# Kernel optimization log

Hardware: AMD Instinct MI355X
Metric: run time of the kernel (lower is better)

## Reference

```python
import jax, jax.numpy as jnp
import numpy as np


def group_norm(x, g, b, groups, eps=1e-5):
    # x: (B, C, H, W), PyTorch GroupNorm semantics
    B, C, H, W = x.shape
    xr = x.reshape(B, groups, -1)
    m = xr.mean(-1, keepdims=True)
    v = xr.var(-1, keepdims=True)
    xn = ((xr - m) * jax.lax.rsqrt(v + eps)).reshape(B, C, H, W)
    return xn * g[:, None, None] + b[:, None, None]


def mamba(xs, in_w, conv_w, conv_b, xproj_w, dt_w, dt_b, A_log, D, out_w):
    # Standard Mamba block: in_proj -> causal depthwise conv -> SiLU ->
    # x_proj -> softplus(dt_proj) -> selective scan -> gate -> out_proj.
    Bsz, L, d = xs.shape
    di = in_w.shape[0] // 2
    r = dt_w.shape[1]
    n = A_log.shape[1]
    K = conv_w.shape[1]
    xz = xs @ in_w.T                           # (B, L, 2*di)
    xpart, z = xz[..., :di], xz[..., di:]
    xp = jnp.pad(xpart, ((0, 0), (K - 1, 0), (0, 0)))  # causal pad
    xc = conv_b + sum(xp[:, k:k + L, :] * conv_w[:, k] for k in range(K))
    xc = jax.nn.silu(xc)
    proj = xc @ xproj_w.T                      # (B, L, r + 2n)
    dt = proj[..., :r]
    Bm = proj[..., r:r + n]
    Cm = proj[..., r + n:]
    delta = jax.nn.softplus(dt @ dt_w.T + dt_b)   # (B, L, di)
    A = -jnp.exp(A_log)                            # (di, n)
    dA = jnp.exp(jnp.einsum('bld,dn->bldn', delta, A))
    dBu = jnp.einsum('bld,bln,bld->bldn', delta, Bm, xc)

    def step(h, inp):
        dA_t, dBu_t, C_t = inp
        h = dA_t * h + dBu_t                  # (B, di, n)
        return h, jnp.einsum('bdn,bn->bd', h, C_t)

    h0 = jnp.zeros((Bsz, di, n), xs.dtype)
    _, ys = jax.lax.scan(step, h0, (jnp.moveaxis(dA, 1, 0), jnp.moveaxis(dBu, 1, 0), jnp.moveaxis(Cm, 1, 0)))
    y = jnp.moveaxis(ys, 0, 1) + D * xc
    y = y * jax.nn.silu(z)
    return y @ out_w.T


def setup_inputs() -> dict:
    def nrm(i, shape, s=0.05):
        return jax.random.normal(jax.random.fold_in(jax.random.key(0), i), shape, dtype=jnp.float32) * s

    f32 = jnp.float32
    C = 128
    di, r, n = 256, 8, 16          # spa mamba: d_model=128, expand=2
    di2, r2 = 64, 2                # spe mamba: d_model=32
    A1 = jnp.log(jnp.broadcast_to(jnp.arange(1, n + 1, dtype=f32), (di, n)))
    A2 = jnp.log(jnp.broadcast_to(jnp.arange(1, n + 1, dtype=f32), (di2, n)))
    return {
        'x': nrm(0, (2, C, 64, 64), 1.0),
        'pe_w': nrm(1, (C, C)), 'pe_b': jnp.zeros((C,), f32),
        'pe_gn_g': jnp.ones((C,), f32), 'pe_gn_b': jnp.zeros((C,), f32),
        'spa_in_w': nrm(2, (2 * di, C)),
        'spa_conv_w': nrm(3, (di, 4)), 'spa_conv_b': jnp.zeros((di,), f32),
        'spa_xproj_w': nrm(4, (r + 2 * n, di)),
        'spa_dt_w': nrm(5, (di, r)), 'spa_dt_b': jnp.full((di,), -2.0, f32),
        'spa_Alog': A1, 'spa_D': jnp.ones((di,), f32),
        'spa_out_w': nrm(6, (C, di)),
        'spa_gn_g': jnp.ones((C,), f32), 'spa_gn_b': jnp.zeros((C,), f32),
        'spe_in_w': nrm(7, (2 * di2, 32)),
        'spe_conv_w': nrm(8, (di2, 4)), 'spe_conv_b': jnp.zeros((di2,), f32),
        'spe_xproj_w': nrm(9, (r2 + 2 * n, di2)),
        'spe_dt_w': nrm(10, (di2, r2)), 'spe_dt_b': jnp.full((di2,), -2.0, f32),
        'spe_Alog': A2, 'spe_D': jnp.ones((di2,), f32),
        'spe_out_w': nrm(11, (32, di2)),
        'spe_gn_g': jnp.ones((C,), f32), 'spe_gn_b': jnp.zeros((C,), f32),
        'fuse_w': jnp.full((2,), 0.5, f32),
        'cls_w': nrm(12, (10, C)), 'cls_b': jnp.zeros((10,), f32),
        'ref_dw_w': nrm(13, (C, 1, 3, 3)),
        'ref_gn_g': jnp.ones((C,), f32), 'ref_gn_b': jnp.zeros((C,), f32),
        'ref_pw_w': nrm(14, (1, C)), 'ref_pw_b': jnp.zeros((1,), f32),
        'alpha': jnp.asarray(1e-4, f32),
    }


def reference(x, pe_w, pe_b, pe_gn_g, pe_gn_b, spa_in_w, spa_conv_w, spa_conv_b, spa_xproj_w, spa_dt_w, spa_dt_b, spa_Alog, spa_D, spa_out_w, spa_gn_g, spa_gn_b, spe_in_w, spe_conv_w, spe_conv_b, spe_xproj_w, spe_dt_w, spe_dt_b, spe_Alog, spe_D, spe_out_w, spe_gn_g, spe_gn_b, fuse_w, cls_w, cls_b, ref_dw_w, ref_gn_g, ref_gn_b, ref_pw_w, ref_pw_b, alpha):
    B, _, H, W = x.shape
    # patch embedding: 1x1 conv + GroupNorm + SiLU
    h1 = jnp.einsum('bchw,oc->bohw', x, pe_w) + pe_b[:, None, None]
    h1 = jax.nn.silu(group_norm(h1, pe_gn_g, pe_gn_b, 4))
    # SpaMamba: scan over flattened spatial tokens (B, H*W, C)
    seq = h1.transpose(0, 2, 3, 1).reshape(B, H * W, -1)
    y = mamba(seq, spa_in_w, spa_conv_w, spa_conv_b, spa_xproj_w, spa_dt_w, spa_dt_b, spa_Alog, spa_D, spa_out_w)
    y = y.reshape(B, H, W, -1).transpose(0, 3, 1, 2)
    spa = jax.nn.silu(group_norm(y, spa_gn_g, spa_gn_b, 4)) + h1
    # SpeMamba: token_num=4, group_channel_num=32, channel_num=128 (no pad)
    seq2 = h1.transpose(0, 2, 3, 1).reshape(B * H * W, 4, 32)
    y2 = mamba(seq2, spe_in_w, spe_conv_w, spe_conv_b, spe_xproj_w, spe_dt_w, spe_dt_b, spe_Alog, spe_D, spe_out_w)
    y2 = y2.reshape(B, H, W, -1).transpose(0, 3, 1, 2)
    spe = h1 + jax.nn.silu(group_norm(y2, spe_gn_g, spe_gn_b, 4))
    # attention-weighted fusion + residual (BothMamba, use_att=True)
    wts = jax.nn.softmax(fuse_w)
    feat = spa * wts[0] + spe * wts[1] + h1
    # classifier head (1x1 conv)
    logits = jnp.einsum('bchw,oc->bohw', feat, cls_w) + cls_b[:, None, None]
    # BoundaryAwareLogitRefiner
    edge = jax.lax.conv_general_dilated(feat, ref_dw_w, (1, 1), ((1, 1), (1, 1)), feature_group_count=feat.shape[1], dimension_numbers=('NCHW', 'OIHW', 'NCHW'))
    edge = jax.nn.silu(group_norm(edge, ref_gn_g, ref_gn_b, 4))
    edge = jax.nn.sigmoid(jnp.einsum('bchw,oc->bohw', edge, ref_pw_w) + ref_pw_b[:, None, None])
    local = jax.lax.reduce_window(logits, 0.0, jax.lax.add, (1, 1, 3, 3), (1, 1, 1, 1), ((0, 0), (0, 0), (1, 1), (1, 1))) / 9.0  # count_include_pad=True
    return logits + alpha * (1.0 - edge) * (local - logits)
```

## Files before the change

### kernel.cpp

```cpp
#include <hip/hip_runtime.h>
#include <math.h>

#define DEV __device__ __forceinline__

DEV float sigm(float x){ return 1.f/(1.f+__expf(-x)); }
DEV float siluf(float x){ return x * sigm(x); }
DEV float softplusf(float x){ return x > 20.f ? x : log1pf(__expf(x)); }

static constexpr float NG = 131072.0f;

static constexpr size_t WS_H1    = 0;
static constexpr size_t WS_H1PRE = 1048576;
static constexpr size_t WS_XC    = 2097152;
static constexpr size_t WS_ZSIL  = 4194304;
static constexpr size_t WS_XZ    = 6291456;
static constexpr size_t WS_LOG   = 8650752;
static constexpr size_t WS_Y     = 10485760;
static constexpr size_t WS_QB    = 12582912;
static constexpr size_t WS_HSB   = 13631488;
static constexpr size_t WS_Y2    = 14155776;
static constexpr size_t WS_FEAT  = 15204352;
static constexpr size_t WS_STATS = 16252928;
static constexpr size_t WS_PEWT  = 16253056;
static constexpr size_t WS_INWT  = WS_PEWT  + 16384;
static constexpr size_t WS_OUTWT = WS_INWT  + 65536;

__global__ void __launch_bounds__(256)
k_red(const float* __restrict__ part, float* __restrict__ outS, int half){
  __shared__ float red[4];
  int b = blockIdx.x >> 3, j = blockIdx.x & 7;
  float s = 0.f;
  for (int i = b*half + threadIdx.x; i < (b+1)*half; i += 256)
    s += part[(size_t)i*8 + j];
  s += __shfl_xor(s,1); s += __shfl_xor(s,2); s += __shfl_xor(s,4);
  s += __shfl_xor(s,8); s += __shfl_xor(s,16); s += __shfl_xor(s,32);
  if ((threadIdx.x & 63) == 0) red[threadIdx.x>>6] = s;
  __syncthreads();
  if (threadIdx.x == 0) outS[b*8+j] = red[0]+red[1]+red[2]+red[3];
}

__global__ void __launch_bounds__(256)
k_transpose(const float* __restrict__ pe_w, const float* __restrict__ in_w,
            const float* __restrict__ out_w,
            float* __restrict__ peT, float* __restrict__ inT,
            float* __restrict__ outT){
  int i0 = blockIdx.x*256 + threadIdx.x;
  int nt = gridDim.x*256;
  for (int k = i0; k < 128*128; k += nt){ int r = k >> 7, c = k & 127; peT[c*128 + r] = pe_w[k]; }
  for (int k = i0; k < 512*128; k += nt){ int r = k >> 7, c = k & 127; inT[c*512 + r] = in_w[k]; }
  for (int k = i0; k < 128*256; k += nt){ int r = k >> 8, c = k & 255; outT[c*128 + r] = out_w[k]; }
}

__global__ void __launch_bounds__(256)
k_pe(const float* __restrict__ x, const float* __restrict__ peT,
     const float* __restrict__ pe_b, float* __restrict__ h1pre,
     float* __restrict__ part){
  __shared__ float As[16][36];
  __shared__ float Bs[16][64];
  __shared__ float red1[2][4], red2[2][4];
  int tid = threadIdx.x;
  int bx = blockIdx.x, by = blockIdx.y;
  int m0 = bx*32, n0 = by*64;
  int b = m0 >> 12, pl0 = m0 & 4095;
  int tx = tid & 15, ty = tid >> 4;
  float acc[2][4];
  #pragma unroll
  for (int i = 0; i < 2; i++)
    #pragma unroll
    for (int j = 0; j < 4; j++) acc[i][j] = 0.f;
  for (int k0 = 0; k0 < 128; k0 += 16){
    if (tid < 128){
      int k = tid >> 3, mm = (tid & 7)*4;
      float4 a = *(const float4*)(x + ((size_t)b*128 + k0+k)*4096 + pl0 + mm);
      *(float4*)&As[k][mm] = a;
    }
    {
      int k = tid >> 4, n = (tid & 15)*4;
      *(float4*)&Bs[k][n] = *(const float4*)(peT + (size_t)(k0+k)*128 + n0+n);
    }
    __syncthreads();
    #pragma unroll
    for (int k = 0; k < 16; k++){
      float2 av = *(const float2*)&As[k][ty*2];
      float4 bv = *(const float4*)&Bs[k][tx*4];
      acc[0][0] += av.x*bv.x; acc[0][1] += av.x*bv.y; acc[0][2] += av.x*bv.z; acc[0][3] += av.x*bv.w;
      acc[1][0] += av.y*bv.x; acc[1][1] += av.y*bv.y; acc[1][2] += av.y*bv.z; acc[1][3] += av.y*bv.w;
    }
    __syncthreads();
  }
  float4 bias = *(const float4*)(pe_b + n0 + tx*4);
  float s1 = 0.f, s2 = 0.f;
  #pragma unroll
  for (int i = 0; i < 2; i++){
    float4 st;
    st.x = acc[i][0]+bias.x; st.y = acc[i][1]+bias.y;
    st.z = acc[i][2]+bias.z; st.w = acc[i][3]+bias.w;
    s1 += st.x+st.y+st.z+st.w;
    s2 += st.x*st.x + st.y*st.y + st.z*st.z + st.w*st.w;
    *(float4*)(h1pre + (size_t)(m0 + ty*2 + i)*128 + n0 + tx*4) = st;
  }
  s1 += __shfl_xor(s1,1);  s2 += __shfl_xor(s2,1);
  s1 += __shfl_xor(s1,2);  s2 += __shfl_xor(s2,2);
  s1 += __shfl_xor(s1,4);  s2 += __shfl_xor(s2,4);
  s1 += __shfl_xor(s1,16); s2 += __shfl_xor(s2,16);
  s1 += __shfl_xor(s1,32); s2 += __shfl_xor(s2,32);
  int lane = tid & 63, w = tid >> 6;
  if ((lane & 55) == 0){
    int gl = (lane >> 3) & 1;
    red1[gl][w] = s1; red2[gl][w] = s2;
  }
  __syncthreads();
  if (tid < 8){
    int gg = tid >> 1, which = tid & 1;
    int gl = gg - by*2;
    float v = 0.f;
    if (gl == 0 || gl == 1){
      v = which ? (red2[gl][0]+red2[gl][1]+red2[gl][2]+red2[gl][3])
                : (red1[gl][0]+red1[gl][1]+red1[gl][2]+red1[gl][3]);
    }
    int pblk = b*256 + (bx & 127) + by*128;
    part[(size_t)pblk*8 + tid] = v;
  }
}

__global__ void __launch_bounds__(256)
k_xz(const float* __restrict__ h1pre, const float* __restrict__ inT,
     const float* __restrict__ stats, const float* __restrict__ gng,
     const float* __restrict__ gnb, float* __restrict__ h1,
     float* __restrict__ xz, float* __restrict__ zsil){
  __shared__ float As[16][68];
  __shared__ float Bs[16][64];
  int tid = threadIdx.x;
  int m0 = blockIdx.x*64, n0 = blockIdx.y*64;
  int tx = tid & 15, ty = tid >> 4;
  float acc[4][4];
  #pragma unroll
  for (int i = 0; i < 4; i++)
    #pragma unroll
    for (int j = 0; j < 4; j++) acc[i][j] = 0.f;
  for (int k0 = 0; k0 < 128; k0 += 16){
    {
      int m = tid >> 2, kk = (tid & 3)*4;
      int pixm = m0 + m, c0 = k0 + kk;
      int bb = pixm >> 12, g = c0 >> 5;
      float4 a = *(const float4*)(h1pre + (size_t)pixm*128 + c0);
      float mu = stats[(bb*4+g)*2] * (1.f/NG);
      float var = stats[(bb*4+g)*2+1] * (1.f/NG) - mu*mu;
      float rs = rsqrtf(var + 1e-5f);
      float4 gg = *(const float4*)(gng + c0);
      float4 gb = *(const float4*)(gnb + c0);
      float4 v;
      v.x = siluf((a.x-mu)*rs*gg.x + gb.x);
      v.y = siluf((a.y-mu)*rs*gg.y + gb.y);
      v.z = siluf((a.z-mu)*rs*gg.z + gb.z);
      v.w = siluf((a.w-mu)*rs*gg.w + gb.w);
      As[kk+0][m] = v.x; As[kk+1][m] = v.y; As[kk+2][m] = v.z; As[kk+3][m] = v.w;
      if (blockIdx.y == 0) *(float4*)(h1 + (size_t)pixm*128 + c0) = v;
    }
    {
      int k = tid >> 4, n = (tid & 15)*4;
      *(float4*)&Bs[k][n] = *(const float4*)(inT + (size_t)(k0+k)*512 + n0+n);
    }
    __syncthreads();
    #pragma unroll
    for (int k = 0; k < 16; k++){
      float4 av = *(const float4*)&As[k][ty*4];
      float4 bv = *(const float4*)&Bs[k][tx*4];
      acc[0][0] += av.x*bv.x; acc[0][1] += av.x*bv.y; acc[0][2] += av.x*bv.z; acc[0][3] += av.x*bv.w;
      acc[1][0] += av.y*bv.x; acc[1][1] += av.y*bv.y; acc[1][2] += av.y*bv.z; acc[1][3] += av.y*bv.w;
      acc[2][0] += av.z*bv.x; acc[2][1] += av.z*bv.y; acc[2][2] += av.z*bv.z; acc[2][3] += av.z*bv.w;
      acc[3][0] += av.w*bv.x; acc[3][1] += av.w*bv.y; acc[3][2] += av.w*bv.z; acc[3][3] += av.w*bv.w;
    }
    __syncthreads();
  }
  if (n0 < 256){
    #pragma unroll
    for (int i = 0; i < 4; i++){
      float4 st; st.x = acc[i][0]; st.y = acc[i][1]; st.z = acc[i][2]; st.w = acc[i][3];
      *(float4*)(xz + (size_t)(m0 + ty*4 + i)*512 + n0 + tx*4) = st;
    }
  } else {
    #pragma unroll
    for (int i = 0; i < 4; i++){
      float4 st;
      st.x = siluf(acc[i][0]); st.y = siluf(acc[i][1]);
      st.z = siluf(acc[i][2]); st.w = siluf(acc[i][3]);
      *(float4*)(zsil + (size_t)(m0 + ty*4 + i)*256 + (n0-256) + tx*4) = st;
    }
  }
}

__global__ void __launch_bounds__(256)
k_conv(const float* __restrict__ xz, const float* __restrict__ cw,
       const float* __restrict__ cb, float* __restrict__ xc){
  int idx = blockIdx.x*256 + threadIdx.x;
  int d = idx & 255;
  int l = (idx >> 8) & 4095;
  int b = idx >> 20;
  float v = cb[d];
  #pragma unroll
  for (int k = 0; k < 4; k++){
    int ls = l - 3 + k;
    if (ls >= 0) v += xz[(size_t)(b*4096 + ls)*512 + d] * cw[d*4 + k];
  }
  xc[idx] = siluf(v);
}

__global__ void __launch_bounds__(256)
k_proj(const float* __restrict__ xc, const float* __restrict__ xpw,
       float* __restrict__ proj){
  __shared__ float As[32][33];
  int tid = threadIdx.x;
  int t = tid & 31;
  int jg = tid >> 5;
  int tok0 = blockIdx.x * 32;
  float acc[5];
  #pragma unroll
  for (int j = 0; j < 5; j++) acc[j] = 0.f;
  for (int k0 = 0; k0 < 256; k0 += 32){
    {
      int m = tid >> 3, kk = (tid & 7)*4;
      float4 a = *(const float4*)(xc + (size_t)(tok0+m)*256 + k0+kk);
      As[kk+0][m]=a.x; As[kk+1][m]=a.y; As[kk+2][m]=a.z; As[kk+3][m]=a.w;
    }
    __syncthreads();
    #pragma unroll
    for (int k4 = 0; k4 < 8; k4++){
      float a0 = As[k4*4+0][t];
      float a1 = As[k4*4+1][t];
      float a2 = As[k4*4+2][t];
      float a3 = As[k4*4+3][t];
      #pragma unroll
      for (int j = 0; j < 5; j++){
        float4 w = *(const float4*)(xpw + (size_t)(jg*5+j)*256 + k0 + k4*4);
        acc[j] += a0*w.x + a1*w.y + a2*w.z + a3*w.w;
      }
    }
    __syncthreads();
  }
  float* pr = proj + (size_t)(tok0+t)*40 + jg*5;
  #pragma unroll
  for (int j = 0; j < 5; j++) pr[j] = acc[j];
}

__global__ void __launch_bounds__(256)
k_scan1(const float* __restrict__ proj, const float* __restrict__ xc,
        const float* __restrict__ dtw, const float* __restrict__ dtb,
        const float* __restrict__ Alog, float* __restrict__ P,
        float* __restrict__ Q){
  int blk = blockIdx.x;
  int dblk = blk & 3;
  int bc = blk >> 2;
  int b = bc >> 7, chunk = bc & 127;
  int tid = threadIdx.x;
  int dl = tid >> 2, ng = tid & 3;
  int d = dblk*64 + dl;
  float4 a4 = *(const float4*)(Alog + (size_t)d*16 + ng*4);
  float An[4] = {-__expf(a4.x), -__expf(a4.y), -__expf(a4.z), -__expf(a4.w)};
  const float4* wr = (const float4*)(dtw + (size_t)d*8);
  float4 w0 = wr[0], w1 = wr[1];
  float bd = dtb[d];
  float Pv[4] = {1.f,1.f,1.f,1.f}, Qv[4] = {0.f,0.f,0.f,0.f};
  size_t row0 = (size_t)(b*4096 + chunk*32);
  for (int l = 0; l < 32; l++){
    size_t r = row0 + l;
    const float4* pr4 = (const float4*)(proj + r*40);
    float4 p0 = pr4[0], p1 = pr4[1];
    float4 bm = pr4[2+ng];
    float dv = softplusf(bd + p0.x*w0.x + p0.y*w0.y + p0.z*w0.z + p0.w*w0.w
                            + p1.x*w1.x + p1.y*w1.y + p1.z*w1.z + p1.w*w1.w);
    float xv = xc[r*256 + d];
    float dBx = dv*xv;
    float bmv[4] = {bm.x, bm.y, bm.z, bm.w};
    #pragma unroll
    for (int k = 0; k < 4; k++){
      float a = __expf(dv*An[k]);
      Qv[k] = a*Qv[k] + bmv[k]*dBx;
      Pv[k] *= a;
    }
  }
  size_t o = (size_t)bc*4096 + dblk*1024 + tid*4;
  float4 pv; pv.x=Pv[0]; pv.y=Pv[1]; pv.z=Pv[2]; pv.w=Pv[3];
  float4 qv; qv.x=Qv[0]; qv.y=Qv[1]; qv.z=Qv[2]; qv.w=Qv[3];
  *(float4*)(P + o) = pv;
  *(float4*)(Q + o) = qv;
}

__global__ void __launch_bounds__(256)
k_scan2(const float* __restrict__ P, const float* __restrict__ Q,
        float* __restrict__ hs){
  __shared__ float Ps[128][33], Qs[128][33];
  int tid = threadIdx.x;
  int b = blockIdx.x >> 7;
  int dn0 = (blockIdx.x & 127) * 32;
  for (int i = tid; i < 128*8; i += 256){
    int ch = i >> 3, c4 = (i & 7)*4;
    size_t g = (size_t)(b*128+ch)*4096 + dn0 + c4;
    float4 p = *(const float4*)(P + g);
    float4 q = *(const float4*)(Q + g);
    Ps[ch][c4]=p.x; Ps[ch][c4+1]=p.y; Ps[ch][c4+2]=p.z; Ps[ch][c4+3]=p.w;
    Qs[ch][c4]=q.x; Qs[ch][c4+1]=q.y; Qs[ch][c4+2]=q.z; Qs[ch][c4+3]=q.w;
  }
  __syncthreads();
  int lane = tid & 63, wv = tid >> 6;
  for (int rep = 0; rep < 8; rep++){
    int c = wv*8 + rep;
    float p0 = Ps[2*lane][c],   q0 = Qs[2*lane][c];
    float p1 = Ps[2*lane+1][c], q1 = Qs[2*lane+1][c];
    float p = p0*p1;
    float q = p1*q0 + q1;
    #pragma unroll
    for (int off = 1; off < 64; off <<= 1){
      float pp = __shfl_up(p, off);
      float qp = __shfl_up(q, off);
      if (lane >= off){ q = p*qp + q; p = p*pp; }
    }
    float hprev = __shfl_up(q, 1);
    if (lane == 0) hprev = 0.f;
    Ps[2*lane][c]   = hprev;
    Ps[2*lane+1][c] = p0*hprev + q0;
  }
  __syncthreads();
  for (int i = tid; i < 128*8; i += 256){
    int ch = i >> 3, c4 = (i & 7)*4;
    size_t g = (size_t)(b*128+ch)*4096 + dn0 + c4;
    float4 h;
    h.x = Ps[ch][c4]; h.y = Ps[ch][c4+1]; h.z = Ps[ch][c4+2]; h.w = Ps[ch][c4+3];
    *(float4*)(hs + g) = h;
  }
}

__global__ void __launch_bounds__(256)
k_scan3(const float* __restrict__ proj, const float* __restrict__ xc,
        const float* __restrict__ zsil, const float* __restrict__ dtw,
        const float* __restrict__ dtb, const float* __restrict__ Alog,
        const float* __restrict__ Dv, const float* __restrict__ hs,
        float* __restrict__ y){
  int blk = blockIdx.x;
  int dblk = blk & 3;
  int bc = blk >> 2;
  int b = bc >> 7, chunk = bc & 127;
  int tid = threadIdx.x;
  int dl = tid >> 2, ng = tid & 3;
  int d = dblk*64 + dl;
  float4 a4 = *(const float4*)(Alog + (size_t)d*16 + ng*4);
  float An[4] = {-__expf(a4.x), -__expf(a4.y), -__expf(a4.z), -__expf(a4.w)};
  const float4* wr = (const float4*)(dtw + (size_t)d*8);
  float4 w0 = wr[0], w1 = wr[1];
  float bd = dtb[d];
  float Dd = Dv[d];
  float h[4];
  {
    size_t o = (size_t)bc*4096 + dblk*1024 + tid*4;
    float4 hv = *(const float4*)(hs + o);
    h[0]=hv.x; h[1]=hv.y; h[2]=hv.z; h[3]=hv.w;
  }
  size_t row0 = (size_t)(b*4096 + chunk*32);
  for (int l = 0; l < 32; l++){
    size_t r = row0 + l;
    const float4* pr4 = (const float4*)(proj + r*40);
    float4 p0 = pr4[0], p1 = pr4[1];
    float4 bm = pr4[2+ng];
    float4 cm = pr4[6+ng];
    float dv = softplusf(bd + p0.x*w0.x + p0.y*w0.y + p0.z*w0.z + p0.w*w0.w
                            + p1.x*w1.x + p1.y*w1.y + p1.z*w1.z + p1.w*w1.w);
    float xv = xc[r*256 + d];
    float dBx = dv*xv;
    float bmv[4] = {bm.x, bm.y, bm.z, bm.w};
    float cmv[4] = {cm.x, cm.y, cm.z, cm.w};
    float ys = 0.f;
    #pragma unroll
    for (int k = 0; k < 4; k++){
      float a = __expf(dv*An[k]);
      h[k] = a*h[k] + bmv[k]*dBx;
      ys += h[k]*cmv[k];
    }
    ys += __shfl_xor(ys, 1);
    ys += __shfl_xor(ys, 2);
    if (ng == 0){
      float zv = zsil[r*256 + d];
      y[r*256 + d] = (ys + Dd*xv) * zv;
    }
  }
}

__global__ void __launch_bounds__(256)
k_outproj(const float* __restrict__ y, const float* __restrict__ outT,
          float* __restrict__ yproj, float* __restrict__ part){
  __shared__ float As[16][36];
  __shared__ float Bs[16][64];
  __shared__ float red1[2][4], red2[2][4];
  int tid = threadIdx.x;
  int bx = blockIdx.x, by = blockIdx.y;
  int m0 = bx*32, n0 = by*64;
  int b = m0 >> 12;
  int tx = tid & 15, ty = tid >> 4;
  float acc[2][4];
  #pragma unroll
  for (int i = 0; i < 2; i++)
    #pragma unroll
    for (int j = 0; j < 4; j++) acc[i][j] = 0.f;
  for (int k0 = 0; k0 < 256; k0 += 16){
    if (tid < 128){
      int m = tid >> 2, kk = (tid & 3)*4;
      float4 a = *(const float4*)(y + (size_t)(m0+m)*256 + k0+kk);
      As[kk+0][m] = a.x; As[kk+1][m] = a.y; As[kk+2][m] = a.z; As[kk+3][m] = a.w;
    }
    {
      int k = tid >> 4, n = (tid & 15)*4;
      *(float4*)&Bs[k][n] = *(const float4*)(outT + (size_t)(k0+k)*128 + n0+n);
    }
    __syncthreads();
    #pragma unroll
    for (int k = 0; k < 16; k++){
      float2 av = *(const float2*)&As[k][ty*2];
      float4 bv = *(const float4*)&Bs[k][tx*4];
      acc[0][0] += av.x*bv.x; acc[0][1] += av.x*bv.y; acc[0][2] += av.x*bv.z; acc[0][3] += av.x*bv.w;
      acc[1][0] += av.y*bv.x; acc[1][1] += av.y*bv.y; acc[1][2] += av.y*bv.z; acc[1][3] += av.y*bv.w;
    }
    __syncthreads();
  }
  float s1 = 0.f, s2 = 0.f;
  #pragma unroll
  for (int i = 0; i < 2; i++){
    float4 st; st.x = acc[i][0]; st.y = acc[i][1]; st.z = acc[i][2]; st.w = acc[i][3];
    s1 += st.x+st.y+st.z+st.w;
    s2 += st.x*st.x + st.y*st.y + st.z*st.z + st.w*st.w;
    *(float4*)(yproj + (size_t)(m0 + ty*2 + i)*128 + n0 + tx*4) = st;
  }
  s1 += __shfl_xor(s1,1);  s2 += __shfl_xor(s2,1);
  s1 += __shfl_xor(s1,2);  s2 += __shfl_xor(s2,2);
  s1 += __shfl_xor(s1,4);  s2 += __shfl_xor(s2,4);
  s1 += __shfl_xor(s1,16); s2 += __shfl_xor(s2,16);
  s1 += __shfl_xor(s1,32); s2 += __shfl_xor(s2,32);
  int lane = tid & 63, w = tid >> 6;
  if ((lane & 55) == 0){
    int gl = (lane >> 3) & 1;
    red1[gl][w] = s1; red2[gl][w] = s2;
  }
  __syncthreads();
  if (tid < 8){
    int gg = tid >> 1, which = tid & 1;
    int gl = gg - by*2;
    float v = 0.f;
    if (gl == 0 || gl == 1){
      v = which ? (red2[gl][0]+red2[gl][1]+red2[gl][2]+red2[gl][3])
                : (red1[gl][0]+red1[gl][1]+red1[gl][2]+red1[gl][3]);
    }
    int pblk = b*256 + (bx & 127) + by*128;
    part[(size_t)pblk*8 + tid] = v;
  }
}

__global__ void __launch_bounds__(256)
k_spe_a(const float* __restrict__ h1, const float* __restrict__ in_w,
        const float* __restrict__ conv_w, const float* __restrict__ conv_b,
        float* __restrict__ xc2, float* __restrict__ xc2T,
        float* __restrict__ zsil2){
  __shared__ float s_in[4][128];
  int tid = threadIdx.x;
  int w = tid >> 6, lane = tid & 63;
  float wx[32], wz[32];
  {
    const float4* rx = (const float4*)(in_w + (size_t)lane*32);
    const float4* rz = (const float4*)(in_w + (size_t)(64+lane)*32);
    #pragma unroll
    for (int k = 0; k < 8; k++){
      float4 a = rx[k]; wx[k*4]=a.x; wx[k*4+1]=a.y; wx[k*4+2]=a.z; wx[k*4+3]=a.w;
      float4 b = rz[k]; wz[k*4]=b.x; wz[k*4+1]=b.y; wz[k*4+2]=b.z; wz[k*4+3]=b.w;
    }
  }
  float4 cwv = ((const float4*)conv_w)[lane];
  float cbv = conv_b[lane];
  for (int i = 0; i < 4; i++){
    int pix = blockIdx.x*16 + w*4 + i;
    float2 hv = ((const float2*)(h1 + (size_t)pix*128))[lane];
    s_in[w][2*lane] = hv.x; s_in[w][2*lane+1] = hv.y;
    float xpr[4], zs[4];
    #pragma unroll
    for (int l = 0; l < 4; l++){
      const float4* sv = (const float4*)&s_in[w][l*32];
      float ax = 0.f, az = 0.f;
      #pragma unroll
      for (int c4 = 0; c4 < 8; c4++){
        float4 v = sv[c4];
        ax += v.x*wx[c4*4] + v.y*wx[c4*4+1] + v.z*wx[c4*4+2] + v.w*wx[c4*4+3];
        az += v.x*wz[c4*4] + v.y*wz[c4*4+1] + v.z*wz[c4*4+2] + v.w*wz[c4*4+3];
      }
      xpr[l] = ax; zs[l] = siluf(az);
    }
    #pragma unroll
    for (int l = 0; l < 4; l++){
      float v = cbv;
      if (l >= 3) v += xpr[l-3]*cwv.x;
      if (l >= 2) v += xpr[l-2]*cwv.y;
      if (l >= 1) v += xpr[l-1]*cwv.z;
      v += xpr[l]*cwv.w;
      float sx = siluf(v);
      int tok = pix*4 + l;
      xc2 [(size_t)tok*64 + lane] = sx;
      xc2T[(size_t)lane*32768 + tok] = sx;
      zsil2[(size_t)tok*64 + lane] = zs[l];
    }
  }
}

__global__ void __launch_bounds__(256)
k_spe_b(const float* __restrict__ xc2T, const float* __restrict__ xpw,
        float* __restrict__ proj){
  int tok = blockIdx.x*256 + threadIdx.x;
  float xcv[64];
  #pragma unroll 64
  for (int dd = 0; dd < 64; dd++) xcv[dd] = xc2T[(size_t)dd*32768 + tok];
  float* pr = proj + (size_t)tok*36;
  #pragma unroll 2
  for (int j = 0; j < 34; j++){
    const float4* wr = (const float4*)(xpw + j*64);
    float a = 0.f;
    #pragma unroll
    for (int k = 0; k < 16; k++){
      float4 wv = wr[k];
      a += xcv[k*4]*wv.x + xcv[k*4+1]*wv.y + xcv[k*4+2]*wv.z + xcv[k*4+3]*wv.w;
    }
    pr[j] = a;
  }
}

__global__ void __launch_bounds__(256)
k_spe_c(const float* __restrict__ xc2, const float* __restrict__ zsil2,
        const float* __restrict__ proj, const float* __restrict__ dt_w,
        const float* __restrict__ dt_b, const float* __restrict__ Alog,
        const float* __restrict__ Dvec, float* __restrict__ yg){
  int tid = threadIdx.x;
  int w = tid >> 6, lane = tid & 63;
  float2 dtwv = ((const float2*)dt_w)[lane];
  float dbv = dt_b[lane], Dd = Dvec[lane];
  float An[16];
  {
    const float4* ar = (const float4*)(Alog + (size_t)lane*16);
    #pragma unroll
    for (int k = 0; k < 4; k++){
      float4 a = ar[k];
      An[k*4]   = -__expf(a.x); An[k*4+1] = -__expf(a.y);
      An[k*4+2] = -__expf(a.z); An[k*4+3] = -__expf(a.w);
    }
  }
  for (int i = 0; i < 4; i++){
    int pix = blockIdx.x*16 + w*4 + i;
    float h[16];
    #pragma unroll
    for (int n = 0; n < 16; n++) h[n] = 0.f;
    #pragma unroll
    for (int l = 0; l < 4; l++){
      int tok = pix*4 + l;
      float pj[36];
      {
        const float4* pr = (const float4*)(proj + (size_t)tok*36);
        #pragma unroll
        for (int k = 0; k < 9; k++){
          float4 v = pr[k];
          pj[k*4]=v.x; pj[k*4+1]=v.y; pj[k*4+2]=v.z; pj[k*4+3]=v.w;
        }
      }
      float xv = xc2[(size_t)tok*64 + lane];
      float zv = zsil2[(size_t)tok*64 + lane];
      float dt = softplusf(dbv + pj[0]*dtwv.x + pj[1]*dtwv.y);
      float ys = 0.f;
      #pragma unroll
      for (int n = 0; n < 16; n++){
        float a = __expf(dt * An[n]);
        h[n] = a*h[n] + dt * pj[2+n] * xv;
        ys += h[n] * pj[18+n];
      }
      yg[(size_t)tok*64 + lane] = (ys + Dd*xv) * zv;
    }
  }
}

__global__ void __launch_bounds__(256)
k_spe_d(const float* __restrict__ yg, const float* __restrict__ out_w,
        float* __restrict__ y2, float* __restrict__ part){
  __shared__ float ldsWT[64*32];
  __shared__ float bst[8];
  int tid = threadIdx.x;
  for (int i = tid; i < 2048; i += 256){
    int c2 = i >> 6, dd = i & 63;
    ldsWT[dd*32 + c2] = out_w[i];
  }
  if (tid < 8) bst[tid] = 0.f;
  __syncthreads();
  int w = tid >> 6, lane = tid & 63;
  int c2 = lane & 31, slot = lane >> 5;
  int tokbase = blockIdx.x*64 + w*16 + slot;
  float acc[8];
  #pragma unroll
  for (int i = 0; i < 8; i++) acc[i] = 0.f;
  for (int dd4 = 0; dd4 < 16; dd4++){
    float w0 = ldsWT[(dd4*4+0)*32 + c2];
    float w1 = ldsWT[(dd4*4+1)*32 + c2];
    float w2 = ldsWT[(dd4*4+2)*32 + c2];
    float w3 = ldsWT[(dd4*4+3)*32 + c2];
    #pragma unroll
    for (int i = 0; i < 8; i++){
      int tok = tokbase + 2*i;
      float4 yv = ((const float4*)(yg + (size_t)tok*64))[dd4];
      acc[i] += yv.x*w0 + yv.y*w1 + yv.z*w2 + yv.w*w3;
    }
  }
  #pragma unroll
  for (int i = 0; i < 8; i++){
    int tok = tokbase + 2*i;
    int pix = tok >> 2, l = tok & 3;
    y2[(size_t)pix*128 + l*32 + c2] = acc[i];
    float s1 = acc[i], s2 = acc[i]*acc[i];
    s1 += __shfl_xor(s1,1);  s2 += __shfl_xor(s2,1);
    s1 += __shfl_xor(s1,2);  s2 += __shfl_xor(s2,2);
    s1 += __shfl_xor(s1,4);  s2 += __shfl_xor(s2,4);
    s1 += __shfl_xor(s1,8);  s2 += __shfl_xor(s2,8);
    s1 += __shfl_xor(s1,16); s2 += __shfl_xor(s2,16);
    if (c2 == 0){
      atomicAdd(&bst[l*2+0], s1);
      atomicAdd(&bst[l*2+1], s2);
    }
  }
  __syncthreads();
  if (tid < 8) part[(size_t)blockIdx.x*8 + tid] = bst[tid];
}

__global__ void __launch_bounds__(256)
k_fuse(const float* __restrict__ h1, const float* __restrict__ yproj,
       const float* __restrict__ y2, const float* __restrict__ stats,
       const float* __restrict__ spa_g, const float* __restrict__ spa_b,
       const float* __restrict__ spe_g, const float* __restrict__ spe_b,
       const float* __restrict__ fuse_w, const float* __restrict__ cls_w,
       const float* __restrict__ cls_b, float* __restrict__ feat,
       float* __restrict__ logits){
  __shared__ float ft[2][128];
  int tid = threadIdx.x;
  int pixl = tid >> 7, c = tid & 127;
  int pix = blockIdx.x*2 + pixl;
  int b = pix >> 12, g = c >> 5;
  float m1 = stats[16 + (b*4+g)*2]   * (1.f/NG);
  float v1 = stats[16 + (b*4+g)*2+1] * (1.f/NG) - m1*m1;
  float m2 = stats[32 + (b*4+g)*2]   * (1.f/NG);
  float v2 = stats[32 + (b*4+g)*2+1] * (1.f/NG) - m2*m2;
  float h = h1[(size_t)pix*128 + c];
  float sa = siluf((yproj[(size_t)pix*128+c] - m1)*rsqrtf(v1+1e-5f)*spa_g[c] + spa_b[c]) + h;
  float sp = h + siluf((y2[(size_t)pix*128+c] - m2)*rsqrtf(v2+1e-5f)*spe_g[c] + spe_b[c]);
  float e0 = __expf(fuse_w[0]), e1 = __expf(fuse_w[1]);
  float w0 = e0/(e0+e1), w1 = e1/(e0+e1);
  float f = sa*w0 + sp*w1 + h;
  feat[(size_t)pix*128+c] = f;
  ft[pixl][c] = f;
  __syncthreads();
  if (tid < 20){
    int pl = (tid >= 10) ? 1 : 0;
    int o = tid - pl*10;
    float acc = cls_b[o];
    for (int cc = 0; cc < 128; cc++) acc += ft[pl][cc]*cls_w[o*128+cc];
    logits[(size_t)(blockIdx.x*2 + pl)*16 + o] = acc;
  }
}

__global__ void __launch_bounds__(256)
k_dw(const float* __restrict__ feat, const float* __restrict__ dww,
     float* __restrict__ epre, float* __restrict__ part){
  __shared__ float red1[4][64], red2[4][64];
  int tid = threadIdx.x;
  int pixl = tid >> 7, c = tid & 127;
  int pix = blockIdx.x*2 + pixl;
  int b = pix >> 12, p = pix & 4095, yy = p >> 6, xx = p & 63;
  float acc = 0.f;
  for (int dy = -1; dy <= 1; dy++){
    int ny = yy + dy; if (ny < 0 || ny > 63) continue;
    for (int dx = -1; dx <= 1; dx++){
      int nx = xx + dx; if (nx < 0 || nx > 63) continue;
      acc += feat[(size_t)((b<<12)|(ny<<6)|nx)*128 + c] * dww[c*9 + (dy+1)*3 + (dx+1)];
    }
  }
  epre[(size_t)pix*128 + c] = acc;
  int g = c >> 5;
  int idx = (c & 31) | (pixl << 5);
  red1[g][idx] = acc; red2[g][idx] = acc*acc;
  __syncthreads();
  int rg = tid >> 6, ridx = tid & 63;
  for (int s = 32; s >= 1; s >>= 1){
    if (ridx < s){ red1[rg][ridx] += red1[rg][ridx+s]; red2[rg][ridx] += red2[rg][ridx+s]; }
    __syncthreads();
  }
  if (ridx == 0){
    part[(size_t)blockIdx.x*8 + rg*2+0] = red1[rg][0];
    part[(size_t)blockIdx.x*8 + rg*2+1] = red2[rg][0];
  }
}

__global__ void __launch_bounds__(256)
k_final(const float* __restrict__ epre, const float* __restrict__ logits,
        const float* __restrict__ stats, const float* __restrict__ rg_g,
        const float* __restrict__ rg_b, const float* __restrict__ pw_w,
        const float* __restrict__ pw_b, const float* __restrict__ alpha,
        float* __restrict__ outp){
  __shared__ float part[4];
  __shared__ float edge_s[2];
  int tid = threadIdx.x;
  int pixl = tid >> 7, c = tid & 127;
  int pix = blockIdx.x*2 + pixl;
  int b = pix >> 12, p = pix & 4095, yy = p >> 6, xx = p & 63;
  int g = c >> 5;
  float m = stats[48 + (b*4+g)*2]   * (1.f/NG);
  float v = stats[48 + (b*4+g)*2+1] * (1.f/NG) - m*m;
  float e = epre[(size_t)pix*128+c];
  float en = siluf((e-m)*rsqrtf(v+1e-5f)*rg_g[c] + rg_b[c]);
  float pv = en * pw_w[c];
  pv += __shfl_xor(pv,1);  pv += __shfl_xor(pv,2);  pv += __shfl_xor(pv,4);
  pv += __shfl_xor(pv,8);  pv += __shfl_xor(pv,16); pv += __shfl_xor(pv,32);
  if ((tid & 63) == 0) part[tid>>6] = pv;
  __syncthreads();
  if (tid < 2) edge_s[tid] = sigm(part[tid*2] + part[tid*2+1] + pw_b[0]);
  __syncthreads();
  if (c < 10){
    float ed = edge_s[pixl];
    int o = c;
    float lg = logits[(size_t)pix*16 + o];
    float loc = 0.f;
    for (int dy = -1; dy <= 1; dy++){
      int ny = yy+dy; if (ny < 0 || ny > 63) continue;
      for (int dx = -1; dx <= 1; dx++){
        int nx = xx+dx; if (nx < 0 || nx > 63) continue;
        loc += logits[(size_t)((b<<12)|(ny<<6)|nx)*16 + o];
      }
    }
    loc *= (1.f/9.f);
    outp[(size_t)((b*10+o)<<12) + p] = lg + alpha[0]*(1.f-ed)*(loc - lg);
  }
}

extern "C" void kernel_launch(void* const* d_in, const int* in_sizes, int n_in,
                              void* d_out, int out_size, void* d_ws, size_t ws_size,
                              hipStream_t stream){
  const float* x          = (const float*)d_in[0];
  const float* pe_w       = (const float*)d_in[1];
  const float* pe_b       = (const float*)d_in[2];
  const float* pe_gn_g    = (const float*)d_in[3];
  const float* pe_gn_b    = (const float*)d_in[4];
  const float* spa_in_w   = (const float*)d_in[5];
  const float* spa_conv_w = (const float*)d_in[6];
  const float* spa_conv_b = (const float*)d_in[7];
  const float* spa_xproj_w= (const float*)d_in[8];
  const float* spa_dt_w   = (const float*)d_in[9];
  const float* spa_dt_b   = (const float*)d_in[10];
  const float* spa_Alog   = (const float*)d_in[11];
  const float* spa_D      = (const float*)d_in[12];
  const float* spa_out_w  = (const float*)d_in[13];
  const float* spa_gn_g   = (const float*)d_in[14];
  const float* spa_gn_b   = (const float*)d_in[15];
  const float* spe_in_w   = (const float*)d_in[16];
  const float* spe_conv_w = (const float*)d_in[17];
  const float* spe_conv_b = (const float*)d_in[18];
  const float* spe_xproj_w= (const float*)d_in[19];
  const float* spe_dt_w   = (const float*)d_in[20];
  const float* spe_dt_b   = (const float*)d_in[21];
  const float* spe_Alog   = (const float*)d_in[22];
  const float* spe_D      = (const float*)d_in[23];
  const float* spe_out_w  = (const float*)d_in[24];
  const float* spe_gn_g   = (const float*)d_in[25];
  const float* spe_gn_b   = (const float*)d_in[26];
  const float* fuse_w     = (const float*)d_in[27];
  const float* cls_w      = (const float*)d_in[28];
  const float* cls_b      = (const float*)d_in[29];
  const float* ref_dw_w   = (const float*)d_in[30];
  const float* ref_gn_g   = (const float*)d_in[31];
  const float* ref_gn_b   = (const float*)d_in[32];
  const float* ref_pw_w   = (const float*)d_in[33];
  const float* ref_pw_b   = (const float*)d_in[34];
  const float* alpha      = (const float*)d_in[35];
  float* ws  = (float*)d_ws;
  float* out = (float*)d_out;

  float* Pb  = ws + WS_H1PRE;
  float* Qb  = ws + WS_QB;
  float* HSb = ws + WS_HSB;
  float* partPE  = ws + WS_Y;
  float* partSPA = ws + WS_QB;
  float* partSPE = ws + WS_QB + 16384;
  float* partDW  = ws + WS_QB + 65536;
  float* proj  = ws + WS_XZ;
  float* xc2   = ws + WS_XC;
  float* xc2T  = ws + WS_ZSIL;
  float* zsil2 = ws + WS_XZ;
  float* proj2 = ws + WS_XZ + 2097152;
  float* yg    = ws + WS_Y;

  k_transpose<<<64,256,0,stream>>>(pe_w, spa_in_w, spa_out_w,
      ws+WS_PEWT, ws+WS_INWT, ws+WS_OUTWT);
  k_pe<<<dim3(256,2),256,0,stream>>>(x, ws+WS_PEWT, pe_b, ws+WS_H1PRE, partPE);
  k_red<<<16,256,0,stream>>>(partPE, ws+WS_STATS+0, 256);
  k_xz<<<dim3(128,8),256,0,stream>>>(ws+WS_H1PRE, ws+WS_INWT, ws+WS_STATS,
      pe_gn_g, pe_gn_b, ws+WS_H1, ws+WS_XZ, ws+WS_ZSIL);
  k_conv<<<8192,256,0,stream>>>(ws+WS_XZ, spa_conv_w, spa_conv_b, ws+WS_XC);
  k_proj<<<256,256,0,stream>>>(ws+WS_XC, spa_xproj_w, proj);
  k_scan1<<<1024,256,0,stream>>>(proj, ws+WS_XC, spa_dt_w, spa_dt_b, spa_Alog,
      Pb, Qb);
  k_scan2<<<256,256,0,stream>>>(Pb, Qb, HSb);
  k_scan3<<<1024,256,0,stream>>>(proj, ws+WS_XC, ws+WS_ZSIL, spa_dt_w, spa_dt_b,
      spa_Alog, spa_D, HSb, ws+WS_Y);
  k_outproj<<<dim3(256,2),256,0,stream>>>(ws+WS_Y, ws+WS_OUTWT, ws+WS_H1PRE, partSPA);
  k_red<<<16,256,0,stream>>>(partSPA, ws+WS_STATS+16, 256);
  k_spe_a<<<512,256,0,stream>>>(ws+WS_H1, spe_in_w, spe_conv_w, spe_conv_b,
      xc2, xc2T, zsil2);
  k_spe_b<<<128,256,0,stream>>>(xc2T, spe_xproj_w, proj2);
  k_spe_c<<<512,256,0,stream>>>(xc2, zsil2, proj2, spe_dt_w, spe_dt_b,
      spe_Alog, spe_D, yg);
  k_spe_d<<<512,256,0,stream>>>(yg, spe_out_w, ws+WS_Y2, partSPE);
  k_red<<<16,256,0,stream>>>(partSPE, ws+WS_STATS+32, 256);
  k_fuse<<<4096,256,0,stream>>>(ws+WS_H1, ws+WS_H1PRE, ws+WS_Y2, ws+WS_STATS,
      spa_gn_g, spa_gn_b, spe_gn_g, spe_gn_b, fuse_w, cls_w, cls_b,
      ws+WS_FEAT, ws+WS_LOG);
  k_dw<<<4096,256,0,stream>>>(ws+WS_FEAT, ref_dw_w, ws+WS_Y, partDW);
  k_red<<<16,256,0,stream>>>(partDW, ws+WS_STATS+48, 2048);
  k_final<<<4096,256,0,stream>>>(ws+WS_Y, ws+WS_LOG, ws+WS_STATS,
      ref_gn_g, ref_gn_b, ref_pw_w, ref_pw_b, alpha, out);
  (void)in_sizes; (void)n_in; (void)out_size; (void)ws_size;
}
```

Measured before the change: 422.9 us.

## Precompute delta once, halve scan chunk length, use exp2 with prescaled A

Adds a k_delta kernel that computes softplus(dt_proj) once per token and channel and writes it to workspace. Before, that projection was recomputed by every state-group thread in both scan passes. The chunked selective scan now uses 16-token chunks instead of 32, which doubles the grid of scan1 and scan3. scan2 is reworked so each lane combines 4 chunks before the wave-level prefix. A is prescaled by log2(e) so the state decay uses exp2f. The trade-off is an extra kernel launch and an extra round trip of the delta tensor through global memory, plus a workspace relayout and an in-place y write that aliases delta.

Measured after the change: 387.7 us. 8.3% less time.

```diff
diff --git a/kernel.cpp b/kernel.cpp
--- a/kernel.cpp
+++ b/kernel.cpp
@@ -8,16 +8,17 @@
 DEV float softplusf(float x){ return x > 20.f ? x : log1pf(__expf(x)); }
 
 static constexpr float NG = 131072.0f;
+static constexpr float LOG2E = 1.4426950408889634f;
 
 static constexpr size_t WS_H1    = 0;
 static constexpr size_t WS_H1PRE = 1048576;
 static constexpr size_t WS_XC    = 2097152;
 static constexpr size_t WS_ZSIL  = 4194304;
 static constexpr size_t WS_XZ    = 6291456;
+static constexpr size_t WS_QOFF  = 6619136;
 static constexpr size_t WS_LOG   = 8650752;
 static constexpr size_t WS_Y     = 10485760;
-static constexpr size_t WS_QB    = 12582912;
-static constexpr size_t WS_HSB   = 13631488;
+static constexpr size_t WS_POFF  = 12582912;
 static constexpr size_t WS_Y2    = 14155776;
 static constexpr size_t WS_FEAT  = 15204352;
 static constexpr size_t WS_STATS = 16252928;
@@ -244,37 +245,54 @@
 }
 
 __global__ void __launch_bounds__(256)
-k_scan1(const float* __restrict__ proj, const float* __restrict__ xc,
-        const float* __restrict__ dtw, const float* __restrict__ dtb,
-        const float* __restrict__ Alog, float* __restrict__ P,
-        float* __restrict__ Q){
+k_delta(const float* __restrict__ proj, const float* __restrict__ dtw,
+        const float* __restrict__ dtb, float* __restrict__ delta){
+  int tid = threadIdx.x;
+  int tok = blockIdx.x*4 + (tid >> 6);
+  int lane = tid & 63;
+  int d0 = lane*4;
+  const float4* pr4 = (const float4*)(proj + (size_t)tok*40);
+  float4 p0 = pr4[0], p1 = pr4[1];
+  float4 outv;
+  float* po = (float*)&outv;
+  #pragma unroll
+  for (int j = 0; j < 4; j++){
+    int d = d0 + j;
+    const float4* wr = (const float4*)(dtw + (size_t)d*8);
+    float4 w0 = wr[0], w1 = wr[1];
+    float v = dtb[d] + p0.x*w0.x + p0.y*w0.y + p0.z*w0.z + p0.w*w0.w
+                     + p1.x*w1.x + p1.y*w1.y + p1.z*w1.z + p1.w*w1.w;
+    po[j] = softplusf(v);
+  }
+  *(float4*)(delta + (size_t)tok*256 + d0) = outv;
+}
+
+__global__ void __launch_bounds__(256)
+k_scan1(const float* __restrict__ delta, const float* __restrict__ proj,
+        const float* __restrict__ xc, const float* __restrict__ Alog,
+        float* __restrict__ P, float* __restrict__ Q){
   int blk = blockIdx.x;
   int dblk = blk & 3;
   int bc = blk >> 2;
-  int b = bc >> 7, chunk = bc & 127;
+  int b = bc >> 8, chunk = bc & 255;
   int tid = threadIdx.x;
   int dl = tid >> 2, ng = tid & 3;
   int d = dblk*64 + dl;
   float4 a4 = *(const float4*)(Alog + (size_t)d*16 + ng*4);
-  float An[4] = {-__expf(a4.x), -__expf(a4.y), -__expf(a4.z), -__expf(a4.w)};
-  const float4* wr = (const float4*)(dtw + (size_t)d*8);
-  float4 w0 = wr[0], w1 = wr[1];
-  float bd = dtb[d];
+  float An[4] = {-__expf(a4.x)*LOG2E, -__expf(a4.y)*LOG2E,
+                 -__expf(a4.z)*LOG2E, -__expf(a4.w)*LOG2E};
   float Pv[4] = {1.f,1.f,1.f,1.f}, Qv[4] = {0.f,0.f,0.f,0.f};
-  size_t row0 = (size_t)(b*4096 + chunk*32);
-  for (int l = 0; l < 32; l++){
+  size_t row0 = (size_t)(b*4096 + chunk*16);
+  for (int l = 0; l < 16; l++){
     size_t r = row0 + l;
-    const float4* pr4 = (const float4*)(proj + r*40);
-    float4 p0 = pr4[0], p1 = pr4[1];
-    float4 bm = pr4[2+ng];
-    float dv = softplusf(bd + p0.x*w0.x + p0.y*w0.y + p0.z*w0.z + p0.w*w0.w
-                            + p1.x*w1.x + p1.y*w1.y + p1.z*w1.z + p1.w*w1.w);
+    float dv = delta[r*256 + d];
     float xv = xc[r*256 + d];
+    float4 bm = *(const float4*)(proj + r*40 + 8 + ng*4);
     float dBx = dv*xv;
     float bmv[4] = {bm.x, bm.y, bm.z, bm.w};
     #pragma unroll
     for (int k = 0; k < 4; k++){
-      float a = __expf(dv*An[k]);
+      float a = exp2f(dv*An[k]);
       Qv[k] = a*Qv[k] + bmv[k]*dBx;
       Pv[k] *= a;
     }
@@ -289,65 +307,71 @@
 __global__ void __launch_bounds__(256)
 k_scan2(const float* __restrict__ P, const float* __restrict__ Q,
         float* __restrict__ hs){
-  __shared__ float Ps[128][33], Qs[128][33];
-  int tid = threadIdx.x;
-  int b = blockIdx.x >> 7;
-  int dn0 = (blockIdx.x & 127) * 32;
-  for (int i = tid; i < 128*8; i += 256){
-    int ch = i >> 3, c4 = (i & 7)*4;
-    size_t g = (size_t)(b*128+ch)*4096 + dn0 + c4;
-    float4 p = *(const float4*)(P + g);
-    float4 q = *(const float4*)(Q + g);
-    Ps[ch][c4]=p.x; Ps[ch][c4+1]=p.y; Ps[ch][c4+2]=p.z; Ps[ch][c4+3]=p.w;
-    Qs[ch][c4]=q.x; Qs[ch][c4+1]=q.y; Qs[ch][c4+2]=q.z; Qs[ch][c4+3]=q.w;
+  __shared__ float Ps[256][17], Qs[256][17];
+  int tid = threadIdx.x;
+  int b = blockIdx.x >> 8;
+  int dn0 = (blockIdx.x & 255) * 16;
+  for (int i = tid; i < 1024; i += 256){
+    int ch = i >> 2, g = (i & 3)*4;
+    size_t gaddr = (size_t)(b*256+ch)*4096 + dn0 + g;
+    float4 p = *(const float4*)(P + gaddr);
+    float4 q = *(const float4*)(Q + gaddr);
+    Ps[ch][g]=p.x; Ps[ch][g+1]=p.y; Ps[ch][g+2]=p.z; Ps[ch][g+3]=p.w;
+    Qs[ch][g]=q.x; Qs[ch][g+1]=q.y; Qs[ch][g+2]=q.z; Qs[ch][g+3]=q.w;
   }
   __syncthreads();
   int lane = tid & 63, wv = tid >> 6;
-  for (int rep = 0; rep < 8; rep++){
-    int c = wv*8 + rep;
-    float p0 = Ps[2*lane][c],   q0 = Qs[2*lane][c];
-    float p1 = Ps[2*lane+1][c], q1 = Qs[2*lane+1][c];
-    float p = p0*p1;
-    float q = p1*q0 + q1;
+  for (int rep = 0; rep < 4; rep++){
+    int c = wv*4 + rep;
+    float p0 = Ps[4*lane+0][c], q0 = Qs[4*lane+0][c];
+    float p1 = Ps[4*lane+1][c], q1 = Qs[4*lane+1][c];
+    float p2 = Ps[4*lane+2][c], q2 = Qs[4*lane+2][c];
+    float p3 = Ps[4*lane+3][c], q3 = Qs[4*lane+3][c];
+    float p = p0, q = q0;
+    q = p1*q + q1; p *= p1;
+    q = p2*q + q2; p *= p2;
+    q = p3*q + q3; p *= p3;
     #pragma unroll
     for (int off = 1; off < 64; off <<= 1){
       float pp = __shfl_up(p, off);
       float qp = __shfl_up(q, off);
       if (lane >= off){ q = p*qp + q; p = p*pp; }
     }
-    float hprev = __shfl_up(q, 1);
-    if (lane == 0) hprev = 0.f;
-    Ps[2*lane][c]   = hprev;
-    Ps[2*lane+1][c] = p0*hprev + q0;
-  }
-  __syncthreads();
-  for (int i = tid; i < 128*8; i += 256){
-    int ch = i >> 3, c4 = (i & 7)*4;
-    size_t g = (size_t)(b*128+ch)*4096 + dn0 + c4;
+    float h0 = __shfl_up(q, 1);
+    if (lane == 0) h0 = 0.f;
+    float h1 = p0*h0 + q0;
+    float h2 = p1*h1 + q1;
+    float h3 = p2*h2 + q2;
+    Ps[4*lane+0][c] = h0;
+    Ps[4*lane+1][c] = h1;
+    Ps[4*lane+2][c] = h2;
+    Ps[4*lane+3][c] = h3;
+  }
+  __syncthreads();
+  for (int i = tid; i < 1024; i += 256){
+    int ch = i >> 2, g = (i & 3)*4;
+    size_t gaddr = (size_t)(b*256+ch)*4096 + dn0 + g;
     float4 h;
-    h.x = Ps[ch][c4]; h.y = Ps[ch][c4+1]; h.z = Ps[ch][c4+2]; h.w = Ps[ch][c4+3];
-    *(float4*)(hs + g) = h;
-  }
-}
-
-__global__ void __launch_bounds__(256)
-k_scan3(const float* __restrict__ proj, const float* __restrict__ xc,
-        const float* __restrict__ zsil, const float* __restrict__ dtw,
-        const float* __restrict__ dtb, const float* __restrict__ Alog,
-        const float* __restrict__ Dv, const float* __restrict__ hs,
-        float* __restrict__ y){
+    h.x = Ps[ch][g]; h.y = Ps[ch][g+1]; h.z = Ps[ch][g+2]; h.w = Ps[ch][g+3];
+    *(float4*)(hs + gaddr) = h;
+  }
+}
+
+__global__ void __launch_bounds__(256)
+k_scan3(const float* __restrict__ delta, const float* __restrict__ proj,
+        const float* __restrict__ xc, const float* __restrict__ zsil,
+        const float* __restrict__ Alog, const float* __restrict__ Dv,
+        const float* __restrict__ hs, float* __restrict__ y){
   int blk = blockIdx.x;
   int dblk = blk & 3;
   int bc = blk >> 2;
-  int b = bc >> 7, chunk = bc & 127;
+  int b = bc >> 8, chunk = bc & 255;
   int tid = threadIdx.x;
   int dl = tid >> 2, ng = tid & 3;
   int d = dblk*64 + dl;
   float4 a4 = *(const float4*)(Alog + (size_t)d*16 + ng*4);
-  float An[4] = {-__expf(a4.x), -__expf(a4.y), -__expf(a4.z), -__expf(a4.w)};
-  const float4* wr = (const float4*)(dtw + (size_t)d*8);
-  float4 w0 = wr[0], w1 = wr[1];
-  float bd = dtb[d];
+  float An[4] = {-__expf(a4.x)*LOG2E, -__expf(a4.y)*LOG2E,
+                 -__expf(a4.z)*LOG2E, -__expf(a4.w)*LOG2E};
   float Dd = Dv[d];
   float h[4];
   {
@@ -355,23 +379,20 @@
     float4 hv = *(const float4*)(hs + o);
     h[0]=hv.x; h[1]=hv.y; h[2]=hv.z; h[3]=hv.w;
   }
-  size_t row0 = (size_t)(b*4096 + chunk*32);
-  for (int l = 0; l < 32; l++){
+  size_t row0 = (size_t)(b*4096 + chunk*16);
+  for (int l = 0; l < 16; l++){
     size_t r = row0 + l;
-    const float4* pr4 = (const float4*)(proj + r*40);
-    float4 p0 = pr4[0], p1 = pr4[1];
-    float4 bm = pr4[2+ng];
-    float4 cm = pr4[6+ng];
-    float dv = softplusf(bd + p0.x*w0.x + p0.y*w0.y + p0.z*w0.z + p0.w*w0.w
-                            + p1.x*w1.x + p1.y*w1.y + p1.z*w1.z + p1.w*w1.w);
+    float dv = delta[r*256 + d];
     float xv = xc[r*256 + d];
+    float4 bm = *(const float4*)(proj + r*40 + 8 + ng*4);
+    float4 cm = *(const float4*)(proj + r*40 + 24 + ng*4);
     float dBx = dv*xv;
     float bmv[4] = {bm.x, bm.y, bm.z, bm.w};
     float cmv[4] = {cm.x, cm.y, cm.z, cm.w};
     float ys = 0.f;
     #pragma unroll
     for (int k = 0; k < 4; k++){
-      float a = __expf(dv*An[k]);
+      float a = exp2f(dv*An[k]);
       h[k] = a*h[k] + bmv[k]*dBx;
       ys += h[k]*cmv[k];
     }
@@ -541,8 +562,8 @@
     #pragma unroll
     for (int k = 0; k < 4; k++){
       float4 a = ar[k];
-      An[k*4]   = -__expf(a.x); An[k*4+1] = -__expf(a.y);
-      An[k*4+2] = -__expf(a.z); An[k*4+3] = -__expf(a.w);
+      An[k*4]   = -__expf(a.x)*LOG2E; An[k*4+1] = -__expf(a.y)*LOG2E;
+      An[k*4+2] = -__expf(a.z)*LOG2E; An[k*4+3] = -__expf(a.w)*LOG2E;
     }
   }
   for (int i = 0; i < 4; i++){
@@ -568,7 +589,7 @@
       float ys = 0.f;
       #pragma unroll
       for (int n = 0; n < 16; n++){
-        float a = __expf(dt * An[n]);
+        float a = exp2f(dt * An[n]);
         h[n] = a*h[n] + dt * pj[2+n] * xv;
         ys += h[n] * pj[18+n];
       }
@@ -777,13 +798,14 @@
   float* ws  = (float*)d_ws;
   float* out = (float*)d_out;
 
-  float* Pb  = ws + WS_H1PRE;
-  float* Qb  = ws + WS_QB;
-  float* HSb = ws + WS_HSB;
+  float* Pb    = ws + WS_POFF;
+  float* Qb    = ws + WS_QOFF;
+  float* HSb   = Pb;
+  float* dely  = ws + WS_Y;
   float* partPE  = ws + WS_Y;
-  float* partSPA = ws + WS_QB;
-  float* partSPE = ws + WS_QB + 16384;
-  float* partDW  = ws + WS_QB + 65536;
+  float* partSPA = ws + WS_POFF;
+  float* partSPE = ws + WS_POFF + 16384;
+  float* partDW  = ws + WS_POFF + 65536;
   float* proj  = ws + WS_XZ;
   float* xc2   = ws + WS_XC;
   float* xc2T  = ws + WS_ZSIL;
@@ -799,12 +821,12 @@
       pe_gn_g, pe_gn_b, ws+WS_H1, ws+WS_XZ, ws+WS_ZSIL);
   k_conv<<<8192,256,0,stream>>>(ws+WS_XZ, spa_conv_w, spa_conv_b, ws+WS_XC);
   k_proj<<<256,256,0,stream>>>(ws+WS_XC, spa_xproj_w, proj);
-  k_scan1<<<1024,256,0,stream>>>(proj, ws+WS_XC, spa_dt_w, spa_dt_b, spa_Alog,
-      Pb, Qb);
-  k_scan2<<<256,256,0,stream>>>(Pb, Qb, HSb);
-  k_scan3<<<1024,256,0,stream>>>(proj, ws+WS_XC, ws+WS_ZSIL, spa_dt_w, spa_dt_b,
-      spa_Alog, spa_D, HSb, ws+WS_Y);
-  k_outproj<<<dim3(256,2),256,0,stream>>>(ws+WS_Y, ws+WS_OUTWT, ws+WS_H1PRE, partSPA);
+  k_delta<<<2048,256,0,stream>>>(proj, spa_dt_w, spa_dt_b, dely);
+  k_scan1<<<2048,256,0,stream>>>(dely, proj, ws+WS_XC, spa_Alog, Pb, Qb);
+  k_scan2<<<512,256,0,stream>>>(Pb, Qb, HSb);
+  k_scan3<<<2048,256,0,stream>>>(dely, proj, ws+WS_XC, ws+WS_ZSIL,
+      spa_Alog, spa_D, HSb, dely );
+  k_outproj<<<dim3(256,2),256,0,stream>>>(dely, ws+WS_OUTWT, ws+WS_H1PRE, partSPA);
   k_red<<<16,256,0,stream>>>(partSPA, ws+WS_STATS+16, 256);
   k_spe_a<<<512,256,0,stream>>>(ws+WS_H1, spe_in_w, spe_conv_w, spe_conv_b,
       xc2, xc2T, zsil2);
```
